# Kernel optimization log

Hardware: AMD Instinct MI355X
Metric: run time of the kernel (lower is better)

The kernel has to match this reference:

```python
import jax, jax.numpy as jnp
import numpy as np

N = 50000       # node_num
E = 800000      # edges (no self loops; reference adds them)
IN_C = 128
OUT_C = 128
HEADS = 1
NEG_SLOPE = 0.2
BN_EPS = 1e-5


def setup_inputs() -> dict:
    key = jax.random.key(0)
    ks = jax.random.split(key, 12)
    x = jax.random.normal(ks[0], (N, IN_C), dtype=jnp.float32)
    # edge_index with no self-loops: dst = (src + off) % N, off in [1, N)
    src = jax.random.randint(ks[1], (E,), 0, N)
    off = jax.random.randint(ks[2], (E,), 1, N)
    dst = (src + off) % N
    edge_index = jnp.stack([src, dst]).astype(jnp.int64)
    embedding = jax.random.normal(ks[3], (N, OUT_C), dtype=jnp.float32)
    s = 1.0 / np.sqrt(IN_C)
    lin_w = jax.random.uniform(ks[4], (HEADS * OUT_C, IN_C), jnp.float32, -s, s)
    g = 0.1
    att_i = jax.random.normal(ks[5], (1, HEADS, OUT_C), jnp.float32) * g
    att_j = jax.random.normal(ks[6], (1, HEADS, OUT_C), jnp.float32) * g
    att_em_i = jax.random.normal(ks[7], (1, HEADS, OUT_C), jnp.float32) * g
    att_em_j = jax.random.normal(ks[8], (1, HEADS, OUT_C), jnp.float32) * g
    bias = jnp.zeros((OUT_C,), jnp.float32)
    gamma = jnp.ones((OUT_C,), jnp.float32)
    beta = jnp.zeros((OUT_C,), jnp.float32)
    return {"x": x, "edge_index": edge_index, "embedding": embedding,
            "lin_w": lin_w, "att_i": att_i, "att_j": att_j,
            "att_em_i": att_em_i, "att_em_j": att_em_j,
            "bias": bias, "gamma": gamma, "beta": beta}


def _gnn_forward(x, embedding, lin_w, att_i, att_j, att_em_i, att_em_j,
                 bias, gamma, beta, src, dst):
    n = x.shape[0]
    xl = (x @ lin_w.T).reshape(n, HEADS, OUT_C)          # [N,H,C]
    x_j = xl[src]                                         # [E',H,C] source
    x_i = xl[dst]                                         # [E',H,C] target
    emb_i = embedding[dst][:, None, :]                    # [E',1,C]
    emb_j = embedding[src][:, None, :]
    # alpha_e = <[x_i||emb_i], [att_i||att_em_i]> + <[x_j||emb_j], [att_j||att_em_j]>
    alpha = ((x_i * att_i).sum(-1) + (emb_i * att_em_i).sum(-1)
             + (x_j * att_j).sum(-1) + (emb_j * att_em_j).sum(-1))  # [E',H]
    alpha = jnp.where(alpha >= 0, alpha, NEG_SLOPE * alpha)         # leaky_relu
    # segment softmax over destination node (PyG softmax)
    amax = jax.ops.segment_max(alpha, dst, num_segments=n)
    ex = jnp.exp(alpha - amax[dst])
    denom = jax.ops.segment_sum(ex, dst, num_segments=n)
    alpha = ex / (denom[dst] + 1e-16)                               # [E',H]
    out = jax.ops.segment_sum(x_j * alpha[..., None], dst, num_segments=n)  # [N,H,C]
    out = out.mean(axis=1) + bias                                   # concat=False
    # BatchNorm1d, training mode (biased batch variance)
    mu = out.mean(axis=0)
    var = ((out - mu) ** 2).mean(axis=0)
    return (out - mu) * jax.lax.rsqrt(var + BN_EPS) * gamma + beta


def reference(x, edge_index, embedding, lin_w, att_i, att_j,
              att_em_i, att_em_j, bias, gamma, beta):
    n = x.shape[0]
    loops = jnp.arange(n, dtype=edge_index.dtype)
    src = jnp.concatenate([edge_index[0], loops])
    dst = jnp.concatenate([edge_index[1], loops])
    return _gnn_forward(x, embedding, lin_w, att_i, att_j, att_em_i,
                        att_em_j, bias, gamma, beta, src, dst)
```

## Files before the change

kernel.cpp:

```cpp
#include <hip/hip_runtime.h>

typedef short bf16x8 __attribute__((ext_vector_type(8)));
typedef float f32x4 __attribute__((ext_vector_type(4)));

__device__ __forceinline__ unsigned short f2bf(float f) {
  unsigned int u = __float_as_uint(f);
  u += 0x7fffu + ((u >> 16) & 1u);
  return (unsigned short)(u >> 16);
}
__device__ __forceinline__ float bf2f(unsigned short h) {
  return __uint_as_float(((unsigned int)h) << 16);
}
__device__ __forceinline__ float lrelu(float a) { return a >= 0.f ? a : 0.2f * a; }

__global__ void zero_kernel(int* __restrict__ p, int n) {
  int i = blockIdx.x * blockDim.x + threadIdx.x;
  int stride = gridDim.x * blockDim.x;
  for (; i < n; i += stride) p[i] = 0;
}

__global__ __launch_bounds__(256) void gemm_cnt_kernel(
    const float* __restrict__ x, const float* __restrict__ w,
    const float* __restrict__ emb,
    const float* __restrict__ att_i, const float* __restrict__ att_j,
    const float* __restrict__ att_em_i, const float* __restrict__ att_em_j,
    unsigned short* __restrict__ xl, float* __restrict__ ai, float* __restrict__ aj,
    int n,
    const int* __restrict__ dst, int* __restrict__ cnt, int* __restrict__ pw, int E,
    int NBG) {
  __shared__ __align__(16) unsigned short xs[64 * 128];
  __shared__ __align__(16) unsigned short wl[128 * 128];
  if (blockIdx.x >= NBG) {
    int e = ((blockIdx.x - NBG) * blockDim.x + threadIdx.x) * 8;
    if (e + 8 <= E) {
      int4 d0 = *(const int4*)(dst + e);
      int4 d1 = *(const int4*)(dst + e + 4);
      int4 p0, p1;
      p0.x = atomicAdd(&cnt[d0.x], 1);
      p0.y = atomicAdd(&cnt[d0.y], 1);
      p0.z = atomicAdd(&cnt[d0.z], 1);
      p0.w = atomicAdd(&cnt[d0.w], 1);
      p1.x = atomicAdd(&cnt[d1.x], 1);
      p1.y = atomicAdd(&cnt[d1.y], 1);
      p1.z = atomicAdd(&cnt[d1.z], 1);
      p1.w = atomicAdd(&cnt[d1.w], 1);
      *(int4*)(pw + e) = p0;
      *(int4*)(pw + e + 4) = p1;
    } else {
      for (; e < E; ++e) pw[e] = atomicAdd(&cnt[dst[e]], 1);
    }
    return;
  }
  const int t = threadIdx.x;
  const int r0 = blockIdx.x * 64;
#pragma unroll
  for (int i = 0; i < 16; ++i) {
    int f4 = t + i * 256;
    int row = f4 >> 5;
    int kk = (f4 & 31) << 2;
    float4 v = *(const float4*)(w + row * 128 + kk);
    ushort4 b;
    b.x = f2bf(v.x); b.y = f2bf(v.y); b.z = f2bf(v.z); b.w = f2bf(v.w);
    int boff = (kk << 1) ^ ((row & 7) << 4);
    *(ushort4*)((char*)wl + row * 256 + boff) = b;
  }
#pragma unroll
  for (int i = 0; i < 8; ++i) {
    int f4 = t + i * 256;
    int row = f4 >> 5;
    int kk = (f4 & 31) << 2;
    int gr = r0 + row;
    float4 v;
    if (gr < n) v = *(const float4*)(x + gr * 128 + kk);
    else { v.x = 0.f; v.y = 0.f; v.z = 0.f; v.w = 0.f; }
    ushort4 b;
    b.x = f2bf(v.x); b.y = f2bf(v.y); b.z = f2bf(v.z); b.w = f2bf(v.w);
    int boff = (kk << 1) ^ ((row & 7) << 4);
    *(ushort4*)((char*)xs + row * 256 + boff) = b;
  }
  __syncthreads();
  const int wid = t >> 6, lane = t & 63;
  const int m16 = lane & 15, kg = lane >> 4;
  const int arow = wid * 16 + m16;
  const f32x4 vzero = {0.f, 0.f, 0.f, 0.f};
  f32x4 acc[8];
#pragma unroll
  for (int i = 0; i < 8; ++i) acc[i] = vzero;
#pragma unroll
  for (int s = 0; s < 4; ++s) {
    int kb = s * 64 + kg * 16;
    bf16x8 a = *(const bf16x8*)((const char*)xs + arow * 256 + (kb ^ ((arow & 7) << 4)));
#pragma unroll
    for (int cf = 0; cf < 8; ++cf) {
      int wrow = cf * 16 + m16;
      bf16x8 b = *(const bf16x8*)((const char*)wl + wrow * 256 + (kb ^ ((wrow & 7) << 4)));
      acc[cf] = __builtin_amdgcn_mfma_f32_16x16x32_bf16(a, b, acc[cf], 0, 0, 0);
    }
  }
  const int crow0 = wid * 16 + kg * 4;
#pragma unroll
  for (int q = 0; q < 4; ++q) {
    int gr = r0 + crow0 + q;
    if (gr < n) {
#pragma unroll
      for (int cf = 0; cf < 8; ++cf)
        xl[gr * 128 + cf * 16 + m16] = f2bf(acc[cf][q]);
    }
  }
  float ati[8], atj[8];
#pragma unroll
  for (int cf = 0; cf < 8; ++cf) {
    ati[cf] = att_i[cf * 16 + m16];
    atj[cf] = att_j[cf * 16 + m16];
  }
  float4 aemi0 = *(const float4*)(att_em_i + m16 * 8);
  float4 aemi1 = *(const float4*)(att_em_i + m16 * 8 + 4);
  float4 aemj0 = *(const float4*)(att_em_j + m16 * 8);
  float4 aemj1 = *(const float4*)(att_em_j + m16 * 8 + 4);
#pragma unroll
  for (int q = 0; q < 4; ++q) {
    int gr = r0 + crow0 + q;
    if (gr < n) {
      float si = 0.f, sj = 0.f;
#pragma unroll
      for (int cf = 0; cf < 8; ++cf) {
        si += acc[cf][q] * ati[cf];
        sj += acc[cf][q] * atj[cf];
      }
      const float* ep = emb + (size_t)gr * 128 + m16 * 8;
      float4 e0 = *(const float4*)(ep);
      float4 e1 = *(const float4*)(ep + 4);
      si += e0.x * aemi0.x + e0.y * aemi0.y + e0.z * aemi0.z + e0.w * aemi0.w
          + e1.x * aemi1.x + e1.y * aemi1.y + e1.z * aemi1.z + e1.w * aemi1.w;
      sj += e0.x * aemj0.x + e0.y * aemj0.y + e0.z * aemj0.z + e0.w * aemj0.w
          + e1.x * aemj1.x + e1.y * aemj1.y + e1.z * aemj1.z + e1.w * aemj1.w;
#pragma unroll
      for (int off = 1; off < 16; off <<= 1) {
        si += __shfl_xor(si, off);
        sj += __shfl_xor(sj, off);
      }
      if (m16 == 0) { ai[gr] = si; aj[gr] = sj; }
    }
  }
}

__global__ __launch_bounds__(1024) void scan1_kernel(
    const int* __restrict__ cnt, int* __restrict__ rp, int* __restrict__ bsum, int n) {
  __shared__ int wsum[16];
  int t = threadIdx.x, lane = t & 63, wid = t >> 6;
  int i = blockIdx.x * 1024 + t;
  int v = (i < n) ? cnt[i] : 0;
  int incl = v;
#pragma unroll
  for (int off = 1; off < 64; off <<= 1) {
    int u = __shfl_up(incl, off);
    if (lane >= off) incl += u;
  }
  if (lane == 63) wsum[wid] = incl;
  __syncthreads();
  if (t < 16) {
    int wv = wsum[t];
    int winc = wv;
#pragma unroll
    for (int off = 1; off < 16; off <<= 1) {
      int u = __shfl_up(winc, off);
      if (t >= off) winc += u;
    }
    wsum[t] = winc - wv;
  }
  __syncthreads();
  int excl = wsum[wid] + incl - v;
  if (i < n) rp[i] = excl;
  if (t == 1023) bsum[blockIdx.x] = excl + v;
}

__global__ __launch_bounds__(256) void scan3_kernel(
    const int* __restrict__ bsum, int* __restrict__ rp, int n, int nb) {
  int lane = threadIdx.x & 63;
  int bb = blockIdx.x >> 2;
  int pref = 0, tot = 0;
  for (int base = 0; base < nb; base += 64) {
    int idx = base + lane;
    int v = (idx < nb) ? bsum[idx] : 0;
    int p = (idx < bb) ? v : 0;
#pragma unroll
    for (int off = 32; off > 0; off >>= 1) {
      p += __shfl_xor(p, off);
      v += __shfl_xor(v, off);
    }
    pref += p;
    tot += v;
  }
  int i = blockIdx.x * 256 + threadIdx.x;
  if (i < n) rp[i] += pref;
  if (blockIdx.x == gridDim.x - 1 && threadIdx.x == 0) rp[n] = tot;
}

__global__ __launch_bounds__(256) void scatter_kernel(
    const int* __restrict__ src, const int* __restrict__ dst,
    const int* __restrict__ rp, const int* __restrict__ pw,
    int* __restrict__ csr, int E) {
  int e = (blockIdx.x * blockDim.x + threadIdx.x) * 8;
  if (e + 8 <= E) {
    int4 s0 = *(const int4*)(src + e);
    int4 s1 = *(const int4*)(src + e + 4);
    int4 d0 = *(const int4*)(dst + e);
    int4 d1 = *(const int4*)(dst + e + 4);
    int4 p0 = *(const int4*)(pw + e);
    int4 p1 = *(const int4*)(pw + e + 4);
    int r0 = rp[d0.x], r1 = rp[d0.y], r2 = rp[d0.z], r3 = rp[d0.w];
    int r4 = rp[d1.x], r5 = rp[d1.y], r6 = rp[d1.z], r7 = rp[d1.w];
    csr[r0 + p0.x] = s0.x;
    csr[r1 + p0.y] = s0.y;
    csr[r2 + p0.z] = s0.z;
    csr[r3 + p0.w] = s0.w;
    csr[r4 + p1.x] = s1.x;
    csr[r5 + p1.y] = s1.y;
    csr[r6 + p1.z] = s1.z;
    csr[r7 + p1.w] = s1.w;
  } else {
    for (; e < E; ++e) csr[rp[dst[e]] + pw[e]] = src[e];
  }
}

__global__ __launch_bounds__(256) void agg_kernel(
    const float* __restrict__ ai, const float* __restrict__ aj,
    const unsigned short* __restrict__ xl,
    const int* __restrict__ row_ptr, const int* __restrict__ csr_src,
    const float* __restrict__ bias, float* __restrict__ out,
    float* __restrict__ pS, float* __restrict__ pQ, int n, int ps2) {
  __shared__ float2 red_s[4][64];
  __shared__ float2 red_q[4][64];
  int wid = threadIdx.x >> 6, lane = threadIdx.x & 63;
  int node = blockIdx.x * 4 + wid;
  bool active = node < n;
  int beg = 0, end = 0;
  float ain = 0.f, w_self = 0.f;
  if (active) {
    beg = row_ptr[node];
    end = row_ptr[node + 1];
    ain = ai[node];
    w_self = __expf(lrelu(ain + aj[node]));
  }
  float dl = 0.f, acc0 = 0.f, acc1 = 0.f;
  const int c0 = lane * 2;
  int s = 0;
  if (beg + lane < end) s = csr_src[beg + lane];
  for (int cs = beg; cs < end; cs += 64) {
    int ce = min(64, end - cs);
    float we = 0.f;
    if (lane < ce) we = __expf(lrelu(ain + aj[s]));
    dl += we;
    int s_nxt = 0;
    if (cs + 64 + lane < end) s_nxt = csr_src[cs + 64 + lane];
    int j = 0;
    for (; j + 8 <= ce; j += 8) {
      float w0 = __shfl(we, j),     w1 = __shfl(we, j + 1);
      float w2 = __shfl(we, j + 2), w3 = __shfl(we, j + 3);
      float w4 = __shfl(we, j + 4), w5 = __shfl(we, j + 5);
      float w6 = __shfl(we, j + 6), w7 = __shfl(we, j + 7);
      int i0 = __shfl(s, j),     i1 = __shfl(s, j + 1);
      int i2 = __shfl(s, j + 2), i3 = __shfl(s, j + 3);
      int i4 = __shfl(s, j + 4), i5 = __shfl(s, j + 5);
      int i6 = __shfl(s, j + 6), i7 = __shfl(s, j + 7);
      ushort2 v0 = *(const ushort2*)(xl + (size_t)i0 * 128 + c0);
      ushort2 v1 = *(const ushort2*)(xl + (size_t)i1 * 128 + c0);
      ushort2 v2 = *(const ushort2*)(xl + (size_t)i2 * 128 + c0);
      ushort2 v3 = *(const ushort2*)(xl + (size_t)i3 * 128 + c0);
      ushort2 v4 = *(const ushort2*)(xl + (size_t)i4 * 128 + c0);
      ushort2 v5 = *(const ushort2*)(xl + (size_t)i5 * 128 + c0);
      ushort2 v6 = *(const ushort2*)(xl + (size_t)i6 * 128 + c0);
      ushort2 v7 = *(const ushort2*)(xl + (size_t)i7 * 128 + c0);
      acc0 += w0 * bf2f(v0.x); acc1 += w0 * bf2f(v0.y);
      acc0 += w1 * bf2f(v1.x); acc1 += w1 * bf2f(v1.y);
      acc0 += w2 * bf2f(v2.x); acc1 += w2 * bf2f(v2.y);
      acc0 += w3 * bf2f(v3.x); acc1 += w3 * bf2f(v3.y);
      acc0 += w4 * bf2f(v4.x); acc1 += w4 * bf2f(v4.y);
      acc0 += w5 * bf2f(v5.x); acc1 += w5 * bf2f(v5.y);
      acc0 += w6 * bf2f(v6.x); acc1 += w6 * bf2f(v6.y);
      acc0 += w7 * bf2f(v7.x); acc1 += w7 * bf2f(v7.y);
    }
    for (; j < ce; ++j) {
      float wj = __shfl(we, j);
      int ij = __shfl(s, j);
      ushort2 v = *(const ushort2*)(xl + (size_t)ij * 128 + c0);
      acc0 += wj * bf2f(v.x); acc1 += wj * bf2f(v.y);
    }
    s = s_nxt;
  }
#pragma unroll
  for (int off = 32; off > 0; off >>= 1) dl += __shfl_xor(dl, off);
  float inv = 1.f / (dl + w_self + 1e-16f);
  float2 o; o.x = 0.f; o.y = 0.f;
  if (active) {
    ushort2 u = *(const ushort2*)(xl + (size_t)node * 128 + c0);
    o.x = (acc0 + w_self * bf2f(u.x)) * inv + bias[c0];
    o.y = (acc1 + w_self * bf2f(u.y)) * inv + bias[c0 + 1];
    *(float2*)(out + (size_t)node * 128 + c0) = o;
  }
  red_s[wid][lane] = o;
  float2 oq; oq.x = o.x * o.x; oq.y = o.y * o.y;
  red_q[wid][lane] = oq;
  __syncthreads();
  int t = threadIdx.x;
  if (t < 128) {
    int l = t >> 1, cm = t & 1;
    float ssum = 0.f;
#pragma unroll
    for (int w = 0; w < 4; ++w) ssum += cm ? red_s[w][l].y : red_s[w][l].x;
    pS[(size_t)t * ps2 + blockIdx.x] = ssum;
  } else {
    int tt = t - 128;
    int l = tt >> 1, cm = tt & 1;
    float qsum = 0.f;
#pragma unroll
    for (int w = 0; w < 4; ++w) qsum += cm ? red_q[w][l].y : red_q[w][l].x;
    pQ[(size_t)tt * ps2 + blockIdx.x] = qsum;
  }
}

__global__ __launch_bounds__(256) void bnstat_b_kernel(
    const float* __restrict__ pS, const float* __restrict__ pQ,
    float* __restrict__ sums, float* __restrict__ sumsq, int nb, int ps2) {
  __shared__ float ws_s[4], ws_q[4];
  int c = blockIdx.x;
  int t = threadIdx.x, lane = t & 63, wid = t >> 6;
  const float* rowS = pS + (size_t)c * ps2;
  const float* rowQ = pQ + (size_t)c * ps2;
  float s = 0.f, qv = 0.f;
  for (int i = t; i < nb; i += 256) {
    s += rowS[i];
    qv += rowQ[i];
  }
#pragma unroll
  for (int off = 32; off > 0; off >>= 1) {
    s += __shfl_xor(s, off);
    qv += __shfl_xor(qv, off);
  }
  if (lane == 0) { ws_s[wid] = s; ws_q[wid] = qv; }
  __syncthreads();
  if (t == 0) {
    sums[c] = ws_s[0] + ws_s[1] + ws_s[2] + ws_s[3];
    sumsq[c] = ws_q[0] + ws_q[1] + ws_q[2] + ws_q[3];
  }
}

__global__ __launch_bounds__(256) void bnapply_kernel(
    float* __restrict__ out, const float* __restrict__ sums,
    const float* __restrict__ sumsq, const float* __restrict__ gamma,
    const float* __restrict__ beta, int n, float invN) {
  int q = threadIdx.x & 31;
  int rs = threadIdx.x >> 5;
  int c = q * 4;
  float4 mu, var, sc, sh;
  mu.x = sums[c + 0] * invN; mu.y = sums[c + 1] * invN;
  mu.z = sums[c + 2] * invN; mu.w = sums[c + 3] * invN;
  var.x = sumsq[c + 0] * invN - mu.x * mu.x;
  var.y = sumsq[c + 1] * invN - mu.y * mu.y;
  var.z = sumsq[c + 2] * invN - mu.z * mu.z;
  var.w = sumsq[c + 3] * invN - mu.w * mu.w;
  sc.x = rsqrtf(var.x + 1e-5f) * gamma[c + 0];
  sc.y = rsqrtf(var.y + 1e-5f) * gamma[c + 1];
  sc.z = rsqrtf(var.z + 1e-5f) * gamma[c + 2];
  sc.w = rsqrtf(var.w + 1e-5f) * gamma[c + 3];
  sh.x = beta[c + 0] - mu.x * sc.x;
  sh.y = beta[c + 1] - mu.y * sc.y;
  sh.z = beta[c + 2] - mu.z * sc.z;
  sh.w = beta[c + 3] - mu.w * sc.w;
  for (int r = blockIdx.x * 8 + rs; r < n; r += gridDim.x * 8) {
    float4 v = *(const float4*)(out + (size_t)r * 128 + c);
    v.x = v.x * sc.x + sh.x;
    v.y = v.y * sc.y + sh.y;
    v.z = v.z * sc.z + sh.z;
    v.w = v.w * sc.w + sh.w;
    *(float4*)(out + (size_t)r * 128 + c) = v;
  }
}

extern "C" void kernel_launch(void* const* d_in, const int* in_sizes, int n_in,
                              void* d_out, int out_size, void* d_ws, size_t ws_size,
                              hipStream_t stream) {
  (void)n_in; (void)out_size; (void)ws_size;
  const float* x = (const float*)d_in[0];
  const int* ei = (const int*)d_in[1];
  const float* emb = (const float*)d_in[2];
  const float* lin_w = (const float*)d_in[3];
  const float* att_i = (const float*)d_in[4];
  const float* att_j = (const float*)d_in[5];
  const float* att_em_i = (const float*)d_in[6];
  const float* att_em_j = (const float*)d_in[7];
  const float* bias = (const float*)d_in[8];
  const float* gamma = (const float*)d_in[9];
  const float* beta = (const float*)d_in[10];
  float* out = (float*)d_out;
  const int N = in_sizes[0] / 128;
  const int E = in_sizes[1] / 2;
  const int* src = ei;
  const int* dst = ei + E;
  const int NB = (N + 1023) / 1024;
  const int NBG = (N + 63) / 64;
  const int NBC = (E / 8 + 255) / 256 + 1;
  const int NBAG = (N + 3) / 4;
  const int PS2 = ((NBAG + 63) / 64) * 64;

  auto align_up = [](size_t v) { return (v + 255) & ~(size_t)255; };
  size_t off = 0;
  size_t xl_off = off;    off = align_up(off + (size_t)N * 128 * 2);
  size_t ai_off = off;    off = align_up(off + (size_t)N * 4);
  size_t aj_off = off;    off = align_up(off + (size_t)N * 4);
  size_t rp_off = off;    off = align_up(off + (size_t)(N + 1) * 4);
  size_t csr_off = off;   off = align_up(off + (size_t)E * 4);
  size_t pw_off = off;    off = align_up(off + (size_t)E * 4);
  size_t bsum_off = off;  off = align_up(off + (size_t)(NB + 1) * 4);
  size_t pS_off = off;    off = align_up(off + (size_t)128 * PS2 * 4);
  size_t pQ_off = off;    off = align_up(off + (size_t)128 * PS2 * 4);
  size_t sums_off = off;  off = align_up(off + 512);
  size_t sumsq_off = off; off = align_up(off + 512);
  size_t cnt_off = off;   off = align_up(off + (size_t)N * 4);

  char* ws = (char*)d_ws;
  unsigned short* xl = (unsigned short*)(ws + xl_off);
  float* ai = (float*)(ws + ai_off);
  float* aj = (float*)(ws + aj_off);
  int* rp = (int*)(ws + rp_off);
  int* csr = (int*)(ws + csr_off);
  int* pw = (int*)(ws + pw_off);
  int* bsum = (int*)(ws + bsum_off);
  float* pS = (float*)(ws + pS_off);
  float* pQ = (float*)(ws + pQ_off);
  float* sums = (float*)(ws + sums_off);
  float* sumsq = (float*)(ws + sumsq_off);
  int* cnt = (int*)(ws + cnt_off);

  hipLaunchKernelGGL(zero_kernel, dim3((N + 255) / 256), dim3(256), 0, stream,
                     cnt, N);
  hipLaunchKernelGGL(gemm_cnt_kernel, dim3(NBG + NBC), dim3(256), 0, stream,
                     x, lin_w, emb, att_i, att_j, att_em_i, att_em_j,
                     xl, ai, aj, N, dst, cnt, pw, E, NBG);
  hipLaunchKernelGGL(scan1_kernel, dim3(NB), dim3(1024), 0, stream, cnt, rp, bsum, N);
  hipLaunchKernelGGL(scan3_kernel, dim3((N + 255) / 256), dim3(256), 0, stream,
                     bsum, rp, N, NB);
  hipLaunchKernelGGL(scatter_kernel, dim3((E / 8 + 255) / 256 + 1), dim3(256), 0,
                     stream, src, dst, rp, pw, csr, E);
  hipLaunchKernelGGL(agg_kernel, dim3(NBAG), dim3(256), 0, stream,
                     ai, aj, xl, rp, csr, bias, out, pS, pQ, N, PS2);
  hipLaunchKernelGGL(bnstat_b_kernel, dim3(128), dim3(256), 0, stream,
                     pS, pQ, sums, sumsq, NBAG, PS2);
  hipLaunchKernelGGL(bnapply_kernel, dim3(2048), dim3(256), 0, stream,
                     out, sums, sumsq, gamma, beta, N, 1.0f / (float)N);
}
```

Before: 265.1 us.

## Store BN partial sums row-major and reduce them in two stages

The aggregation kernel now writes per-block BatchNorm partial sums as contiguous 128-float rows instead of a column-strided layout, so each block's stores are coalesced. The single-stage per-channel reduction is replaced by a 128-block first pass over row chunks, followed by a one-block final pass over 128 rows. This targets uncoalesced strided writes in the aggregation kernel and gives the reduction more parallelism, at the cost of one extra kernel launch and an extra intermediate buffer.

```diff
diff --git a/kernel.cpp b/kernel.cpp
--- a/kernel.cpp
+++ b/kernel.cpp
@@ -228,7 +228,7 @@
     const unsigned short* __restrict__ xl,
     const int* __restrict__ row_ptr, const int* __restrict__ csr_src,
     const float* __restrict__ bias, float* __restrict__ out,
-    float* __restrict__ pS, float* __restrict__ pQ, int n, int ps2) {
+    float* __restrict__ pS, float* __restrict__ pQ, int n) {
   __shared__ float2 red_s[4][64];
   __shared__ float2 red_q[4][64];
   int wid = threadIdx.x >> 6, lane = threadIdx.x & 63;
@@ -308,40 +308,52 @@
     float ssum = 0.f;
 #pragma unroll
     for (int w = 0; w < 4; ++w) ssum += cm ? red_s[w][l].y : red_s[w][l].x;
-    pS[(size_t)t * ps2 + blockIdx.x] = ssum;
+    pS[(size_t)blockIdx.x * 128 + t] = ssum;
   } else {
     int tt = t - 128;
     int l = tt >> 1, cm = tt & 1;
     float qsum = 0.f;
 #pragma unroll
     for (int w = 0; w < 4; ++w) qsum += cm ? red_q[w][l].y : red_q[w][l].x;
-    pQ[(size_t)tt * ps2 + blockIdx.x] = qsum;
-  }
-}
-
-__global__ __launch_bounds__(256) void bnstat_b_kernel(
+    pQ[(size_t)blockIdx.x * 128 + tt] = qsum;
+  }
+}
+
+__global__ __launch_bounds__(256) void bn_b1_kernel(
     const float* __restrict__ pS, const float* __restrict__ pQ,
-    float* __restrict__ sums, float* __restrict__ sumsq, int nb, int ps2) {
-  __shared__ float ws_s[4], ws_q[4];
-  int c = blockIdx.x;
-  int t = threadIdx.x, lane = t & 63, wid = t >> 6;
-  const float* rowS = pS + (size_t)c * ps2;
-  const float* rowQ = pQ + (size_t)c * ps2;
+    float* __restrict__ p2S, float* __restrict__ p2Q, int nb) {
+  __shared__ float comb[2][128];
+  int t = threadIdx.x;
+  int c = t & 127, half = t >> 7;
+  int chunk = (nb + gridDim.x - 1) / gridDim.x;
+  int start = blockIdx.x * chunk;
+  int end = min(nb, start + chunk);
   float s = 0.f, qv = 0.f;
-  for (int i = t; i < nb; i += 256) {
-    s += rowS[i];
-    qv += rowQ[i];
-  }
-#pragma unroll
-  for (int off = 32; off > 0; off >>= 1) {
-    s += __shfl_xor(s, off);
-    qv += __shfl_xor(qv, off);
-  }
-  if (lane == 0) { ws_s[wid] = s; ws_q[wid] = qv; }
-  __syncthreads();
-  if (t == 0) {
-    sums[c] = ws_s[0] + ws_s[1] + ws_s[2] + ws_s[3];
-    sumsq[c] = ws_q[0] + ws_q[1] + ws_q[2] + ws_q[3];
+  for (int r = start + half; r < end; r += 2) {
+    s += pS[(size_t)r * 128 + c];
+    qv += pQ[(size_t)r * 128 + c];
+  }
+  comb[half][c] = s;
+  __syncthreads();
+  if (t < 128) p2S[(size_t)blockIdx.x * 128 + t] = comb[0][t] + comb[1][t];
+  __syncthreads();
+  comb[half][c] = qv;
+  __syncthreads();
+  if (t >= 128) p2Q[(size_t)blockIdx.x * 128 + (t - 128)] = comb[0][t - 128] + comb[1][t - 128];
+}
+
+__global__ __launch_bounds__(256) void bn_b2_kernel(
+    const float* __restrict__ p2S, const float* __restrict__ p2Q,
+    float* __restrict__ sums, float* __restrict__ sumsq, int nb2) {
+  int t = threadIdx.x;
+  int c = t & 127;
+  float acc = 0.f;
+  if (t < 128) {
+    for (int r = 0; r < nb2; ++r) acc += p2S[(size_t)r * 128 + c];
+    sums[c] = acc;
+  } else {
+    for (int r = 0; r < nb2; ++r) acc += p2Q[(size_t)r * 128 + c];
+    sumsq[c] = acc;
   }
 }
 
@@ -401,7 +413,7 @@
   const int NBG = (N + 63) / 64;
   const int NBC = (E / 8 + 255) / 256 + 1;
   const int NBAG = (N + 3) / 4;
-  const int PS2 = ((NBAG + 63) / 64) * 64;
+  const int NB1 = 128;
 
   auto align_up = [](size_t v) { return (v + 255) & ~(size_t)255; };
   size_t off = 0;
@@ -412,8 +424,10 @@
   size_t csr_off = off;   off = align_up(off + (size_t)E * 4);
   size_t pw_off = off;    off = align_up(off + (size_t)E * 4);
   size_t bsum_off = off;  off = align_up(off + (size_t)(NB + 1) * 4);
-  size_t pS_off = off;    off = align_up(off + (size_t)128 * PS2 * 4);
-  size_t pQ_off = off;    off = align_up(off + (size_t)128 * PS2 * 4);
+  size_t pS_off = off;    off = align_up(off + (size_t)NBAG * 128 * 4);
+  size_t pQ_off = off;    off = align_up(off + (size_t)NBAG * 128 * 4);
+  size_t p2S_off = off;   off = align_up(off + (size_t)NB1 * 128 * 4);
+  size_t p2Q_off = off;   off = align_up(off + (size_t)NB1 * 128 * 4);
   size_t sums_off = off;  off = align_up(off + 512);
   size_t sumsq_off = off; off = align_up(off + 512);
   size_t cnt_off = off;   off = align_up(off + (size_t)N * 4);
@@ -428,6 +442,8 @@
   int* bsum = (int*)(ws + bsum_off);
   float* pS = (float*)(ws + pS_off);
   float* pQ = (float*)(ws + pQ_off);
+  float* p2S = (float*)(ws + p2S_off);
+  float* p2Q = (float*)(ws + p2Q_off);
   float* sums = (float*)(ws + sums_off);
   float* sumsq = (float*)(ws + sumsq_off);
   int* cnt = (int*)(ws + cnt_off);
@@ -443,9 +459,11 @@
   hipLaunchKernelGGL(scatter_kernel, dim3((E / 8 + 255) / 256 + 1), dim3(256), 0,
                      stream, src, dst, rp, pw, csr, E);
   hipLaunchKernelGGL(agg_kernel, dim3(NBAG), dim3(256), 0, stream,
-                     ai, aj, xl, rp, csr, bias, out, pS, pQ, N, PS2);
-  hipLaunchKernelGGL(bnstat_b_kernel, dim3(128), dim3(256), 0, stream,
-                     pS, pQ, sums, sumsq, NBAG, PS2);
+                     ai, aj, xl, rp, csr, bias, out, pS, pQ, N);
+  hipLaunchKernelGGL(bn_b1_kernel, dim3(NB1), dim3(256), 0, stream,
+                     pS, pQ, p2S, p2Q, NBAG);
+  hipLaunchKernelGGL(bn_b2_kernel, dim3(1), dim3(256), 0, stream,
+                     p2S, p2Q, sums, sumsq, NB1);
   hipLaunchKernelGGL(bnapply_kernel, dim3(2048), dim3(256), 0, stream,
                      out, sums, sumsq, gamma, beta, N, 1.0f / (float)N);
 }
```

After: 267.7 us. No clear change (+1.0%).
